# Kernel tuning notes

Hardware: AMD Instinct MI355X
Metric: run time of the kernel (lower is better)

The kernel has to match this reference:

```python
import jax, jax.numpy as jnp
from jax import lax
import numpy as np

N, B, P, D, DOUT, MAXDEG = 81920, 4096, 20, 128, 256, 8
EPS = 1e-5

def _bn(x, g, b):
    m = x.mean(0)
    v = x.var(0)
    return (x - m) / jnp.sqrt(v + EPS) * g + b

def setup_inputs() -> dict:
    key = jax.random.key(0)
    ks = jax.random.split(key, 24)
    s = 0.05
    return {
        'feat': jax.random.normal(ks[0], (N, D), jnp.float32),
        'intend': jax.random.normal(ks[1], (B, D), jnp.float32),
        'position_weight': jax.random.uniform(ks[2], (N,), jnp.float32),
        'nbr_idx': jax.random.randint(ks[3], (N, MAXDEG), 0, N),
        'deg': jax.random.randint(ks[4], (N,), 0, MAXDEG + 1),
        'last_nodes': jax.random.randint(ks[5], (B,), 0, N),
        # EOPA params
        'bn1_g': jnp.ones((D,), jnp.float32),
        'bn1_b': jnp.zeros((D,), jnp.float32),
        'W_ih': jax.random.normal(ks[6], (3 * D, D), jnp.float32) * s,
        'W_hh': jax.random.normal(ks[7], (3 * D, D), jnp.float32) * s,
        'b_ih': jax.random.normal(ks[8], (3 * D,), jnp.float32) * s,
        'b_hh': jax.random.normal(ks[9], (3 * D,), jnp.float32) * s,
        'W_self': jax.random.normal(ks[10], (D, D), jnp.float32) * s,
        'W_neigh': jax.random.normal(ks[11], (D, D), jnp.float32) * s,
        # AttnReadout params (hidden_dim == D)
        'bn2_g': jnp.ones((D,), jnp.float32),
        'bn2_b': jnp.zeros((D,), jnp.float32),
        'Wu': jax.random.normal(ks[12], (D, D), jnp.float32) * s,
        'Wv': jax.random.normal(ks[13], (D, D), jnp.float32) * s,
        'bv': jax.random.normal(ks[14], (D,), jnp.float32) * s,
        'Wi': jax.random.normal(ks[15], (D, D), jnp.float32) * s,
        'bi': jax.random.normal(ks[16], (D,), jnp.float32) * s,
        'We': jax.random.normal(ks[17], (D, 1), jnp.float32) * s,
        'Wout': jax.random.normal(ks[18], (DOUT, D), jnp.float32) * s,
    }

def reference(feat, intend, position_weight, nbr_idx, deg, last_nodes,
              bn1_g, bn1_b, W_ih, W_hh, b_ih, b_hh, W_self, W_neigh,
              bn2_g, bn2_b, Wu, Wv, bv, Wi, bi, We, Wout):
    # ---- EOPA: gather mailbox -> GRU over neighbors -> self + neigh mix ----
    h0 = _bn(feat, bn1_g, bn1_b)              # BatchNorm1d (batch stats)
    mail = h0[nbr_idx]                        # [N, MAXDEG, D] gather
    xs = jnp.moveaxis(mail, 0, 1)             # [MAXDEG, N, D]

    def gru_step(h, tx):
        t, x = tx
        gi = x @ W_ih.T + b_ih                # [N, 3D]
        gh = h @ W_hh.T + b_hh
        ir, iz, inn = jnp.split(gi, 3, axis=1)
        hr, hz, hn = jnp.split(gh, 3, axis=1)
        r = jax.nn.sigmoid(ir + hr)
        z = jax.nn.sigmoid(iz + hz)
        n = jnp.tanh(inn + r * hn)
        h_new = (1.0 - z) * n + z * h
        # freeze state past each node's true mailbox length (ragged GRU)
        h = jnp.where((t < deg)[:, None], h_new, h)
        return h, None

    neigh, _ = lax.scan(gru_step, jnp.zeros((N, D), feat.dtype),
                        (jnp.arange(MAXDEG), xs))
    rst = h0 @ W_self.T + neigh @ W_neigh.T   # [N, D], activation=None

    # ---- AttnReadout: segment softmax attention + segment sums ----
    h = _bn(rst, bn2_g, bn2_b)
    fu = (h @ Wu.T).reshape(B, P, D)
    fv = (intend @ Wv.T + bv)[:, None, :]         # broadcast_nodes
    fl = (h[last_nodes] @ Wi.T + bi)[:, None, :]  # broadcast_nodes
    e = (jax.nn.sigmoid(fu + fv + fl) @ We)[..., 0]   # [B, P]
    alpha = jax.nn.softmax(e, axis=1)[..., None]      # segment_softmax
    hg = h.reshape(B, P, D)
    rst_g = (hg * alpha).sum(axis=1) @ Wout.T         # segment_sum + fc_out
    pos = (hg * position_weight.reshape(B, P, 1)).sum(axis=1) @ Wout.T
    return rst_g, pos
```

## Files before the change

kernel.cpp:

```cpp
#include <hip/hip_runtime.h>

#define NN      81920
#define BB      4096
#define PP      20
#define DD      128
#define DOUTT   256
#define MAXDEGG 8
#define NBLK_H  320

using bf16x8 = __attribute__((ext_vector_type(8))) short;
using f32x4  = __attribute__((ext_vector_type(4))) float;
using u16x4  = __attribute__((ext_vector_type(4))) ushort;

__device__ __forceinline__ float b2f(ushort u) {
    union { unsigned u; float f; } v; v.u = ((unsigned)u) << 16; return v.f;
}
__device__ __forceinline__ ushort f2b(float f) {
    union { float f; unsigned u; } v; v.f = f;
    unsigned r = v.u + 0x7fffu + ((v.u >> 16) & 1u);
    return (ushort)(r >> 16);
}
__device__ __forceinline__ float sigm(float x) {
    return __fdividef(1.f, 1.f + __expf(-x));
}
__device__ __forceinline__ float tanh_fast(float x) {
    return 1.f - __fdividef(2.f, 1.f + __expf(2.f * x));
}
__device__ __forceinline__ f32x4 mfma16(bf16x8 a, bf16x8 b, f32x4 c) {
    return __builtin_amdgcn_mfma_f32_16x16x32_bf16(a, b, c, 0, 0, 0);
}
__device__ __forceinline__ bf16x8 pack8(float4 a, float4 b) {
    bf16x8 r;
    r[0] = (short)f2b(a.x); r[1] = (short)f2b(a.y);
    r[2] = (short)f2b(a.z); r[3] = (short)f2b(a.w);
    r[4] = (short)f2b(b.x); r[5] = (short)f2b(b.y);
    r[6] = (short)f2b(b.z); r[7] = (short)f2b(b.w);
    return r;
}
__device__ __forceinline__ bf16x8 ld8_bf(const ushort* p) { return *(const bf16x8*)p; }
__device__ __forceinline__ bf16x8 ld8_f32(const float* p) {
    return pack8(*(const float4*)p, *(const float4*)(p + 4));
}

__global__ __launch_bounds__(256) void stats_hist_k(const float* __restrict__ X,
                                                    const int* __restrict__ deg,
                                                    float* __restrict__ part,
                                                    int* __restrict__ blockHist) {
    const int tid = threadIdx.x;
    if (blockIdx.x < 640) {
        const int col  = tid & 127;
        const int half = tid >> 7;
        const long base = (long)blockIdx.x * 128 + (long)half * 64;
        float s = 0.f, q = 0.f;
        for (int i = 0; i < 64; ++i) {
            float x = X[(base + i) * 128 + col];
            s += x; q += x * x;
        }
        __shared__ float red[2][2][128];
        red[0][half][col] = s;
        red[1][half][col] = q;
        __syncthreads();
        if (tid < 128) {
            part[blockIdx.x * 128 + tid]             = red[0][0][tid] + red[0][1][tid];
            part[640 * 128 + blockIdx.x * 128 + tid] = red[1][0][tid] + red[1][1][tid];
        }
    } else {
        __shared__ int wh[4][9];
        const int hb = blockIdx.x - 640;
        const int w = tid >> 6, lane = tid & 63;
        int d = deg[hb * 256 + tid]; d = min(max(d, 0), 8);
#pragma unroll
        for (int c = 0; c < 9; ++c) {
            unsigned long long m = __ballot(d == c);
            if (lane == 0) wh[w][c] = __popcll(m);
        }
        __syncthreads();
        if (tid < 9) {
            int s = 0;
#pragma unroll
            for (int w2 = 0; w2 < 4; ++w2) s += wh[w2][tid];
            blockHist[hb * 9 + tid] = s;
        }
    }
}

__global__ __launch_bounds__(256) void bnfinal_scan_k(const float* __restrict__ part, int nparts,
                                                      const float* __restrict__ g,
                                                      const float* __restrict__ b,
                                                      float2* __restrict__ ss,
                                                      const int* __restrict__ blockHist,
                                                      int* __restrict__ blockBase) {
    const int t = threadIdx.x;
    if (blockIdx.x < 128) {
        const int c = blockIdx.x;
        float s = 0.f, q = 0.f;
        for (int i = t; i < nparts; i += 256) {
            s += part[(long)i * 128 + c];
            q += part[(long)(nparts + i) * 128 + c];
        }
#pragma unroll
        for (int off = 32; off > 0; off >>= 1) {
            s += __shfl_xor(s, off, 64);
            q += __shfl_xor(q, off, 64);
        }
        __shared__ float rs[4], rq[4];
        if ((t & 63) == 0) { rs[t >> 6] = s; rq[t >> 6] = q; }
        __syncthreads();
        if (t == 0) {
            s = rs[0] + rs[1] + rs[2] + rs[3];
            q = rq[0] + rq[1] + rq[2] + rq[3];
            const float inv_n = 1.f / (float)NN;
            float mean = s * inv_n;
            float var  = q * inv_n - mean * mean;
            float rstd = rsqrtf(var + 1e-5f);
            float sc = g[c] * rstd;
            ss[c] = make_float2(sc, b[c] - mean * sc);
        }
    } else {
        __shared__ int classTot[9], classStart[9];
        if (t < 9) {
            int s = 0;
            for (int b2 = 0; b2 < NBLK_H; ++b2) s += blockHist[b2 * 9 + t];
            classTot[t] = s;
        }
        __syncthreads();
        if (t == 0) {
            int acc = 0;
            for (int k = 0; k < 9; ++k) { classStart[k] = acc; acc += classTot[k]; }
        }
        __syncthreads();
        if (t < 9) {
            int acc = classStart[t];
            for (int b2 = 0; b2 < NBLK_H; ++b2) {
                blockBase[b2 * 9 + t] = acc;
                acc += blockHist[b2 * 9 + t];
            }
        }
    }
}

__global__ __launch_bounds__(256) void scatter_k(const int* __restrict__ deg,
                                                 const int* __restrict__ blockBase,
                                                 int* __restrict__ perm) {
    __shared__ int wh[4][9];
    __shared__ int wbase[4][9];
    const int t = threadIdx.x, w = t >> 6, lane = t & 63;
    const int i = blockIdx.x * 256 + t;
    int d = deg[i]; d = min(max(d, 0), 8);
    int lt = 0;
#pragma unroll
    for (int c = 0; c < 9; ++c) {
        unsigned long long m = __ballot(d == c);
        if (lane == 0) wh[w][c] = __popcll(m);
        if (d == c) lt = __popcll(m & ((1ull << lane) - 1ull));
    }
    __syncthreads();
    if (t < 36) {
        const int w2 = t / 9, c = t - w2 * 9;
        int s = blockBase[blockIdx.x * 9 + c];
        for (int k = 0; k < w2; ++k) s += wh[k][c];
        wbase[w2][c] = s;
    }
    __syncthreads();
    perm[wbase[w][d] + lt] = i;
}

template <int NCOL, int NWAVE, int KPARTS, bool A1F32, bool GATHER2, bool BIAS1,
          bool BIAS2, bool FOLD1, bool FOLD2, int OUTMODE>
__global__ __launch_bounds__(NWAVE * 64) void gemm_bt(
    const void* __restrict__ A1, const void* __restrict__ A2,
    const float* __restrict__ W1, const float* __restrict__ W2,
    const float* __restrict__ bias1, const float* __restrict__ bias2, int blim,
    const float2* __restrict__ ssW1, const float2* __restrict__ ssW2,
    const int* __restrict__ gidx, void* __restrict__ outv,
    float* __restrict__ part, int nparts,
    const float* __restrict__ fvl, const float* __restrict__ We,
    float* __restrict__ e) {
    constexpr int JT = NCOL / (16 * NWAVE);
    __shared__ float epart[8][64];
    const int tid = threadIdx.x;
    const int w   = tid >> 6;
    const int l   = tid & 63;
    const int l15 = l & 15;
    const int l4  = l >> 4;
    const int colbase = w * (NCOL / NWAVE);

    bf16x8 bfr[JT][KPARTS * 4];
    float bv[JT];
    float Wec[JT];
#pragma unroll
    for (int jl = 0; jl < JT; ++jl) {
        const int wrow = colbase + jl * 16 + l15;
        float fb = 0.f;
#pragma unroll
        for (int kp = 0; kp < KPARTS; ++kp) {
            const float* Wp = (kp == 0) ? W1 : W2;
            const float2* sp = (kp == 0) ? ssW1 : ssW2;
            const bool fold = (kp == 0) ? FOLD1 : FOLD2;
#pragma unroll
            for (int kt = 0; kt < 4; ++kt) {
                const float* wp = &Wp[(long)wrow * 128 + kt * 32 + l4 * 8];
                float4 a = *(const float4*)wp;
                float4 b4 = *(const float4*)(wp + 4);
                if (fold) {
                    const float* s = (const float*)(sp + kt * 32 + l4 * 8);
                    float4 s0 = *(const float4*)s, s1 = *(const float4*)(s + 4);
                    float4 s2 = *(const float4*)(s + 8), s3 = *(const float4*)(s + 12);
                    fb += s0.y * a.x + s0.w * a.y + s1.y * a.z + s1.w * a.w
                        + s2.y * b4.x + s2.w * b4.y + s3.y * b4.z + s3.w * b4.w;
                    a.x *= s0.x; a.y *= s0.z; a.z *= s1.x; a.w *= s1.z;
                    b4.x *= s2.x; b4.y *= s2.z; b4.z *= s3.x; b4.w *= s3.z;
                }
                bfr[jl][kp * 4 + kt] = pack8(a, b4);
            }
        }
        if (FOLD1 || FOLD2) {
            fb += __shfl_xor(fb, 16, 64);
            fb += __shfl_xor(fb, 32, 64);
        }
        if (BIAS1) fb += bias1[wrow];
        if (BIAS2) fb += (wrow < blim) ? bias2[wrow] : 0.f;
        bv[jl] = fb;
        if (OUTMODE == 3) Wec[jl] = We[wrow];
    }

    const int rowblk = blockIdx.x * 64;
    const f32x4 fz = {0.f, 0.f, 0.f, 0.f};
    float ssum[JT], sq[JT];
#pragma unroll
    for (int jl = 0; jl < JT; ++jl) { ssum[jl] = 0.f; sq[jl] = 0.f; }

#pragma unroll
    for (int it = 0; it < 4; ++it) {
        const int arow1 = rowblk + it * 16 + l15;
        bf16x8 afr[KPARTS * 4];
#pragma unroll
        for (int kt = 0; kt < 4; ++kt) {
            if (A1F32)
                afr[kt] = ld8_f32(&((const float*)A1)[(long)arow1 * 128 + kt * 32 + l4 * 8]);
            else
                afr[kt] = ld8_bf(&((const ushort*)A1)[(long)arow1 * 128 + kt * 32 + l4 * 8]);
        }
        if (KPARTS == 2) {
            const long arow2 = GATHER2 ? (long)gidx[arow1] : (long)arow1;
#pragma unroll
            for (int kt = 0; kt < 4; ++kt)
                afr[4 + kt] = ld8_bf(&((const ushort*)A2)[arow2 * 128 + kt * 32 + l4 * 8]);
        }
        f32x4 acc[JT];
#pragma unroll
        for (int jl = 0; jl < JT; ++jl) {
            acc[jl] = fz;
#pragma unroll
            for (int kk = 0; kk < KPARTS * 4; ++kk)
                acc[jl] = mfma16(afr[kk], bfr[jl][kk], acc[jl]);
        }
        float ps[4] = {0.f, 0.f, 0.f, 0.f};
#pragma unroll
        for (int jl = 0; jl < JT; ++jl) {
            const int col = colbase + jl * 16 + l15;
#pragma unroll
            for (int r = 0; r < 4; ++r) {
                const long orow = rowblk + it * 16 + l4 * 4 + r;
                float v = acc[jl][r] + bv[jl];
                if (OUTMODE == 0 || OUTMODE == 2)
                    ((ushort*)outv)[orow * NCOL + col] = f2b(v);
                if (OUTMODE == 1)
                    ((float*)outv)[orow * NCOL + col] = v;
                if (OUTMODE == 2) { ssum[jl] += v; sq[jl] += v * v; }
                if (OUTMODE == 3) {
                    const int b = (int)orow / PP;
                    ps[r] += sigm(v + fvl[(long)b * 128 + col]) * Wec[jl];
                }
            }
        }
        if (OUTMODE == 3) {
#pragma unroll
            for (int r = 0; r < 4; ++r) {
#pragma unroll
                for (int off = 1; off < 16; off <<= 1)
                    ps[r] += __shfl_xor(ps[r], off, 64);
            }
            if (l15 == 0) {
#pragma unroll
                for (int r = 0; r < 4; ++r)
                    epart[w][it * 16 + l4 * 4 + r] = ps[r];
            }
        }
    }
    if (OUTMODE == 2) {
#pragma unroll
        for (int jl = 0; jl < JT; ++jl) {
            float s = ssum[jl], q = sq[jl];
            s += __shfl_xor(s, 16, 64); s += __shfl_xor(s, 32, 64);
            q += __shfl_xor(q, 16, 64); q += __shfl_xor(q, 32, 64);
            if (l4 == 0) {
                const int col = colbase + jl * 16 + l15;
                part[(long)blockIdx.x * 128 + col] = s;
                part[(long)nparts * 128 + (long)blockIdx.x * 128 + col] = q;
            }
        }
    }
    if (OUTMODE == 3) {
        __syncthreads();
        if (tid < 64) {
            float s = 0.f;
#pragma unroll
            for (int w2 = 0; w2 < NWAVE; ++w2) s += epart[w2][tid];
            e[rowblk + tid] = s;
        }
    }
}

#define GLOAD(d0, d1, d2, ROW, TT)                                 \
    { const ushort* Gp_ = G + (long)nbrs[ROW][TT] * 384;           \
      d0 = *(const u16x4*)&Gp_[c0];                                \
      d1 = *(const u16x4*)&Gp_[c0 + 128];                          \
      d2 = *(const u16x4*)&Gp_[c0 + 256]; }

#define GRU_STEP(IT, Gv0, Gv1, Gv2)                                         \
    {                                                                       \
        const int row_ = (IT) * 16 + l15;                                   \
        const bool upd_ = (t < dreg[IT]);                                   \
        bf16x8 af0 = *(const bf16x8*)&hbuf[cur][row_][0 * 32 + l4 * 8];     \
        bf16x8 af1 = *(const bf16x8*)&hbuf[cur][row_][1 * 32 + l4 * 8];     \
        bf16x8 af2 = *(const bf16x8*)&hbuf[cur][row_][2 * 32 + l4 * 8];     \
        bf16x8 af3 = *(const bf16x8*)&hbuf[cur][row_][3 * 32 + l4 * 8];     \
        f32x4 ar = fz, az = fz, an = fz;                                    \
        ar = mfma16(bfr[0][0], af0, ar); az = mfma16(bfr[1][0], af0, az);   \
        an = mfma16(bfr[2][0], af0, an);                                    \
        ar = mfma16(bfr[0][1], af1, ar); az = mfma16(bfr[1][1], af1, az);   \
        an = mfma16(bfr[2][1], af1, an);                                    \
        ar = mfma16(bfr[0][2], af2, ar); az = mfma16(bfr[1][2], af2, az);   \
        an = mfma16(bfr[2][2], af2, an);                                    \
        ar = mfma16(bfr[0][3], af3, ar); az = mfma16(bfr[1][3], af3, az);   \
        an = mfma16(bfr[2][3], af3, an);                                    \
        const u16x4 hold_ = *(const u16x4*)&hbuf[cur][row_][c0];            \
        u16x4 hnew_;                                                        \
        _Pragma("unroll")                                                   \
        for (int r = 0; r < 4; ++r) {                                       \
            const float rr = sigm(b2f(Gv0[r]) + ar[r]);                     \
            const float zz = sigm(b2f(Gv1[r]) + az[r]);                     \
            const float nn = tanh_fast(b2f(Gv2[r]) + rr * (an[r] + bnN[r]));\
            const float hv = (1.f - zz) * nn + zz * b2f(hold_[r]);          \
            hnew_[r] = upd_ ? f2b(hv) : hold_[r];                           \
        }                                                                   \
        *(u16x4*)&hbuf[1 - cur][row_][c0] = hnew_;                          \
    }

__global__ __attribute__((amdgpu_flat_work_group_size(512, 512), amdgpu_waves_per_eu(4, 8)))
void gru_kernel(const ushort* __restrict__ G,
                const float* __restrict__ Whh,
                const float* __restrict__ bhh,
                const int* __restrict__ nbr_idx,
                const int* __restrict__ deg,
                const int* __restrict__ perm,
                ushort* __restrict__ neigh) {
    __shared__ alignas(16) ushort hbuf[2][64][136];
    __shared__ alignas(16) int nbrs[64][8];
    __shared__ int degs[64];
    __shared__ int nid[64];

    const int tid = threadIdx.x;
    const int l   = tid & 63;
    const int l15 = l & 15;
    const int l4  = l >> 4;
    const int blockRow = (gridDim.x - 1 - blockIdx.x) * 64;
    const int colbase = (tid >> 6) * 16;
    const int c0 = colbase + l4 * 4;

    if (tid < 64) nid[tid] = perm[blockRow + tid];
    {
        bf16x8 z = {0, 0, 0, 0, 0, 0, 0, 0};
        bf16x8* p = (bf16x8*)&hbuf[0][0][0];
        for (int i = tid; i < 64 * 136 / 8; i += 512) p[i] = z;
    }
    __syncthreads();
    nbrs[tid >> 3][tid & 7] = nbr_idx[(long)nid[tid >> 3] * 8 + (tid & 7)];
    if (tid < 64) degs[tid] = deg[nid[tid]];

    bf16x8 bfr[3][4];
#pragma unroll
    for (int g = 0; g < 3; ++g)
#pragma unroll
        for (int kt = 0; kt < 4; ++kt)
            bfr[g][kt] = ld8_f32(&Whh[(long)(g * 128 + colbase + l15) * 128 + kt * 32 + l4 * 8]);
    const f32x4 bnN = *(const f32x4*)&bhh[256 + c0];
    __syncthreads();

    int dreg[4];
#pragma unroll
    for (int it = 0; it < 4; ++it) dreg[it] = degs[it * 16 + l15];
    int dmax = degs[l];
#pragma unroll
    for (int off = 32; off > 0; off >>= 1) dmax = max(dmax, __shfl_xor(dmax, off, 64));
    dmax = __builtin_amdgcn_readfirstlane(dmax);

    const f32x4 fz = {0.f, 0.f, 0.f, 0.f};
    u16x4 p00, p01, p02, p10, p11, p12;
    GLOAD(p00, p01, p02, l15, 0);
    GLOAD(p10, p11, p12, 16 + l15, 0);

    int cur = 0;
    for (int t = 0; t < dmax; ++t) {
        u16x4 q20, q21, q22, q30, q31, q32;
        GLOAD(q20, q21, q22, 32 + l15, t);
        GLOAD(q30, q31, q32, 48 + l15, t);
        GRU_STEP(0, p00, p01, p02);
        GRU_STEP(1, p10, p11, p12);
        if (t + 1 < dmax) {
            GLOAD(p00, p01, p02, l15, t + 1);
            GLOAD(p10, p11, p12, 16 + l15, t + 1);
        }
        GRU_STEP(2, q20, q21, q22);
        GRU_STEP(3, q30, q31, q32);
        __syncthreads();
        cur ^= 1;
    }
    for (int idx = tid; idx < 64 * 16; idx += 512) {
        const int row = idx >> 4, ch = idx & 15;
        bf16x8* dst = (bf16x8*)(neigh + (long)nid[row] * 128);
        dst[ch] = *(const bf16x8*)&hbuf[cur][row][ch * 8];
    }
}

__global__ __launch_bounds__(256) void seg_k(const ushort* __restrict__ rst,
                                             const float* __restrict__ e,
                                             const float* __restrict__ pw,
                                             const float2* __restrict__ ss2,
                                             ushort* __restrict__ s12) {
    const int g = blockIdx.x * 2 + (threadIdx.x >> 7);
    const int c = threadIdx.x & 127;
    const float2 sc = ss2[c];
    float ev[PP];
    float m = -1e30f;
#pragma unroll
    for (int p = 0; p < PP; ++p) { ev[p] = e[g * PP + p]; m = fmaxf(m, ev[p]); }
    float sum = 0.f;
#pragma unroll
    for (int p = 0; p < PP; ++p) { ev[p] = __expf(ev[p] - m); sum += ev[p]; }
    const float inv = __fdividef(1.f, sum);
    float a1 = 0.f, a2 = 0.f;
#pragma unroll
    for (int p = 0; p < PP; ++p) {
        const int node = g * PP + p;
        const float hv = b2f(rst[(long)node * 128 + c]) * sc.x + sc.y;
        a1 += (ev[p] * inv) * hv;
        a2 += pw[node] * hv;
    }
    s12[(long)g * 128 + c]        = f2b(a1);
    s12[(long)(BB + g) * 128 + c] = f2b(a2);
}

extern "C" void kernel_launch(void* const* d_in, const int* in_sizes, int n_in,
                              void* d_out, int out_size, void* d_ws, size_t ws_size,
                              hipStream_t stream) {
    const float* feat    = (const float*)d_in[0];
    const float* intend  = (const float*)d_in[1];
    const float* pw      = (const float*)d_in[2];
    const int*   nbr_idx = (const int*)d_in[3];
    const int*   deg     = (const int*)d_in[4];
    const int*   last    = (const int*)d_in[5];
    const float* bn1_g   = (const float*)d_in[6];
    const float* bn1_b   = (const float*)d_in[7];
    const float* W_ih    = (const float*)d_in[8];
    const float* W_hh    = (const float*)d_in[9];
    const float* b_ih    = (const float*)d_in[10];
    const float* b_hh    = (const float*)d_in[11];
    const float* W_self  = (const float*)d_in[12];
    const float* W_neigh = (const float*)d_in[13];
    const float* bn2_g   = (const float*)d_in[14];
    const float* bn2_b   = (const float*)d_in[15];
    const float* Wu      = (const float*)d_in[16];
    const float* Wv      = (const float*)d_in[17];
    const float* bv      = (const float*)d_in[18];
    const float* Wi      = (const float*)d_in[19];
    const float* bi      = (const float*)d_in[20];
    const float* We      = (const float*)d_in[21];
    const float* Wout    = (const float*)d_in[22];
    float* out = (float*)d_out;
    char* ws = (char*)d_ws;

    ushort* G     = (ushort*)(ws + 0L);
    ushort* rst   = G;
    ushort* neigh = (ushort*)(ws + 62914560L);
    float*  fvl   = (float*)(ws + 83886080L);
    float*  e     = (float*)(ws + 85983232L);
    ushort* s12   = (ushort*)(ws + 86310912L);
    float*  part1 = (float*)(ws + 88408064L);
    float*  part2 = (float*)(ws + 89063424L);
    int*    perm  = (int*)(ws + 90374144L);
    float2* ss1   = (float2*)(ws + 90701824L);
    float2* ss2   = (float2*)(ws + 90702848L);
    int*    blockHist = (int*)(ws + 90703872L);
    int*    blockBase = (int*)(ws + 90715392L);

    stats_hist_k<<<960, 256, 0, stream>>>(feat, deg, part1, blockHist);
    bnfinal_scan_k<<<129, 256, 0, stream>>>(part1, 640, bn1_g, bn1_b, ss1,
                                            blockHist, blockBase);
    scatter_k<<<NBLK_H, 256, 0, stream>>>(deg, blockBase, perm);

    gemm_bt<384, 4, 1, true, false, true, true, true, false, 0><<<1280, 256, 0, stream>>>(
        feat, nullptr, W_ih, nullptr, b_ih, b_hh, 256, ss1, nullptr,
        nullptr, G, nullptr, 0, nullptr, nullptr, nullptr);

    gru_kernel<<<1280, 512, 0, stream>>>(G, W_hh, b_hh, nbr_idx, deg, perm, neigh);

    gemm_bt<128, 4, 2, true, false, false, false, true, false, 2><<<1280, 256, 0, stream>>>(
        feat, neigh, W_self, W_neigh, nullptr, nullptr, 0, ss1, nullptr,
        nullptr, rst, part2, 1280, nullptr, nullptr, nullptr);
    bnfinal_scan_k<<<128, 256, 0, stream>>>(part2, 1280, bn2_g, bn2_b, ss2,
                                            nullptr, nullptr);

    gemm_bt<128, 4, 2, true, true, true, true, false, true, 1><<<64, 256, 0, stream>>>(
        intend, rst, Wv, Wi, bv, bi, 128, nullptr, ss2,
        last, fvl, nullptr, 0, nullptr, nullptr, nullptr);

    gemm_bt<128, 4, 1, false, false, false, false, true, false, 3><<<1280, 256, 0, stream>>>(
        rst, nullptr, Wu, nullptr, nullptr, nullptr, 0, ss2, nullptr,
        nullptr, nullptr, nullptr, 0, fvl, We, e);

    seg_k<<<2048, 256, 0, stream>>>(rst, e, pw, ss2, s12);

    gemm_bt<256, 4, 1, false, false, false, false, false, false, 1><<<128, 256, 0, stream>>>(
        s12, nullptr, Wout, nullptr, nullptr, nullptr, 0, nullptr, nullptr,
        nullptr, out, nullptr, 0, nullptr, nullptr, nullptr);

    (void)in_sizes; (void)n_in; (void)out_size; (void)ws_size;
}
```

Measured before the change: 329.3 us.

## Fuse attention-score GEMM with segment softmax and weighted sums

Replaces the separate Wu GEMM kernel (which wrote per-node attention scores e) and the segment-reduction kernel with one kernel. Each block computes scores for 80 nodes (4 graphs), does the softmax in shared memory, then computes the attention-weighted and position-weighted sums. This removes a launch, the e buffer round trip, and gives the second rst read a chance to hit cache. In exchange the softmax is done serially by 4 threads, and each block has less parallelism per graph.

```diff
diff --git a/kernel.cpp b/kernel.cpp
--- a/kernel.cpp
+++ b/kernel.cpp
@@ -173,11 +173,8 @@
     const float* __restrict__ bias1, const float* __restrict__ bias2, int blim,
     const float2* __restrict__ ssW1, const float2* __restrict__ ssW2,
     const int* __restrict__ gidx, void* __restrict__ outv,
-    float* __restrict__ part, int nparts,
-    const float* __restrict__ fvl, const float* __restrict__ We,
-    float* __restrict__ e) {
+    float* __restrict__ part, int nparts) {
     constexpr int JT = NCOL / (16 * NWAVE);
-    __shared__ float epart[8][64];
     const int tid = threadIdx.x;
     const int w   = tid >> 6;
     const int l   = tid & 63;
@@ -187,7 +184,6 @@
 
     bf16x8 bfr[JT][KPARTS * 4];
     float bv[JT];
-    float Wec[JT];
 #pragma unroll
     for (int jl = 0; jl < JT; ++jl) {
         const int wrow = colbase + jl * 16 + l15;
@@ -221,7 +217,6 @@
         if (BIAS1) fb += bias1[wrow];
         if (BIAS2) fb += (wrow < blim) ? bias2[wrow] : 0.f;
         bv[jl] = fb;
-        if (OUTMODE == 3) Wec[jl] = We[wrow];
     }
 
     const int rowblk = blockIdx.x * 64;
@@ -255,7 +250,6 @@
             for (int kk = 0; kk < KPARTS * 4; ++kk)
                 acc[jl] = mfma16(afr[kk], bfr[jl][kk], acc[jl]);
         }
-        float ps[4] = {0.f, 0.f, 0.f, 0.f};
 #pragma unroll
         for (int jl = 0; jl < JT; ++jl) {
             const int col = colbase + jl * 16 + l15;
@@ -268,23 +262,6 @@
                 if (OUTMODE == 1)
                     ((float*)outv)[orow * NCOL + col] = v;
                 if (OUTMODE == 2) { ssum[jl] += v; sq[jl] += v * v; }
-                if (OUTMODE == 3) {
-                    const int b = (int)orow / PP;
-                    ps[r] += sigm(v + fvl[(long)b * 128 + col]) * Wec[jl];
-                }
-            }
-        }
-        if (OUTMODE == 3) {
-#pragma unroll
-            for (int r = 0; r < 4; ++r) {
-#pragma unroll
-                for (int off = 1; off < 16; off <<= 1)
-                    ps[r] += __shfl_xor(ps[r], off, 64);
-            }
-            if (l15 == 0) {
-#pragma unroll
-                for (int r = 0; r < 4; ++r)
-                    epart[w][it * 16 + l4 * 4 + r] = ps[r];
             }
         }
     }
@@ -299,15 +276,6 @@
                 part[(long)blockIdx.x * 128 + col] = s;
                 part[(long)nparts * 128 + (long)blockIdx.x * 128 + col] = q;
             }
-        }
-    }
-    if (OUTMODE == 3) {
-        __syncthreads();
-        if (tid < 64) {
-            float s = 0.f;
-#pragma unroll
-            for (int w2 = 0; w2 < NWAVE; ++w2) s += epart[w2][tid];
-            e[rowblk + tid] = s;
         }
     }
 }
@@ -424,32 +392,120 @@
     }
 }
 
-__global__ __launch_bounds__(256) void seg_k(const ushort* __restrict__ rst,
-                                             const float* __restrict__ e,
-                                             const float* __restrict__ pw,
-                                             const float2* __restrict__ ss2,
-                                             ushort* __restrict__ s12) {
-    const int g = blockIdx.x * 2 + (threadIdx.x >> 7);
-    const int c = threadIdx.x & 127;
-    const float2 sc = ss2[c];
-    float ev[PP];
-    float m = -1e30f;
-#pragma unroll
-    for (int p = 0; p < PP; ++p) { ev[p] = e[g * PP + p]; m = fmaxf(m, ev[p]); }
-    float sum = 0.f;
-#pragma unroll
-    for (int p = 0; p < PP; ++p) { ev[p] = __expf(ev[p] - m); sum += ev[p]; }
-    const float inv = __fdividef(1.f, sum);
-    float a1 = 0.f, a2 = 0.f;
-#pragma unroll
-    for (int p = 0; p < PP; ++p) {
-        const int node = g * PP + p;
-        const float hv = b2f(rst[(long)node * 128 + c]) * sc.x + sc.y;
-        a1 += (ev[p] * inv) * hv;
-        a2 += pw[node] * hv;
-    }
-    s12[(long)g * 128 + c]        = f2b(a1);
-    s12[(long)(BB + g) * 128 + c] = f2b(a2);
+__global__ __launch_bounds__(256) void seg_e_k(const ushort* __restrict__ rst,
+                                               const float* __restrict__ Wu,
+                                               const float2* __restrict__ ss2,
+                                               const float* __restrict__ fvl,
+                                               const float* __restrict__ We,
+                                               const float* __restrict__ pw,
+                                               ushort* __restrict__ s12) {
+    __shared__ float epart[4][80];
+    __shared__ float ash[80];
+    const int tid = threadIdx.x;
+    const int w   = tid >> 6;
+    const int l   = tid & 63;
+    const int l15 = l & 15;
+    const int l4  = l >> 4;
+    const int colbase = w * 32;
+    const int rowblk = blockIdx.x * 80;
+
+    bf16x8 bfr[2][4];
+    float bv[2], Wec[2];
+#pragma unroll
+    for (int jl = 0; jl < 2; ++jl) {
+        const int wrow = colbase + jl * 16 + l15;
+        float fb = 0.f;
+#pragma unroll
+        for (int kt = 0; kt < 4; ++kt) {
+            const float* wp = &Wu[(long)wrow * 128 + kt * 32 + l4 * 8];
+            float4 a = *(const float4*)wp;
+            float4 b4 = *(const float4*)(wp + 4);
+            const float* s = (const float*)(ss2 + kt * 32 + l4 * 8);
+            float4 s0 = *(const float4*)s, s1 = *(const float4*)(s + 4);
+            float4 s2 = *(const float4*)(s + 8), s3 = *(const float4*)(s + 12);
+            fb += s0.y * a.x + s0.w * a.y + s1.y * a.z + s1.w * a.w
+                + s2.y * b4.x + s2.w * b4.y + s3.y * b4.z + s3.w * b4.w;
+            a.x *= s0.x; a.y *= s0.z; a.z *= s1.x; a.w *= s1.z;
+            b4.x *= s2.x; b4.y *= s2.z; b4.z *= s3.x; b4.w *= s3.z;
+            bfr[jl][kt] = pack8(a, b4);
+        }
+        fb += __shfl_xor(fb, 16, 64);
+        fb += __shfl_xor(fb, 32, 64);
+        bv[jl] = fb;
+        Wec[jl] = We[wrow];
+    }
+
+    const f32x4 fz = {0.f, 0.f, 0.f, 0.f};
+#pragma unroll
+    for (int it = 0; it < 5; ++it) {
+        const int arow = rowblk + it * 16 + l15;
+        bf16x8 afr[4];
+#pragma unroll
+        for (int kt = 0; kt < 4; ++kt)
+            afr[kt] = ld8_bf(&rst[(long)arow * 128 + kt * 32 + l4 * 8]);
+        f32x4 acc[2];
+#pragma unroll
+        for (int jl = 0; jl < 2; ++jl) {
+            acc[jl] = fz;
+#pragma unroll
+            for (int kt = 0; kt < 4; ++kt)
+                acc[jl] = mfma16(afr[kt], bfr[jl][kt], acc[jl]);
+        }
+        float ps[4] = {0.f, 0.f, 0.f, 0.f};
+#pragma unroll
+        for (int jl = 0; jl < 2; ++jl) {
+            const int col = colbase + jl * 16 + l15;
+#pragma unroll
+            for (int r = 0; r < 4; ++r) {
+                const long orow = rowblk + it * 16 + l4 * 4 + r;
+                const float v = acc[jl][r] + bv[jl];
+                const int bg = (int)orow / PP;
+                ps[r] += sigm(v + fvl[(long)bg * 128 + col]) * Wec[jl];
+            }
+        }
+#pragma unroll
+        for (int r = 0; r < 4; ++r) {
+#pragma unroll
+            for (int off = 1; off < 16; off <<= 1)
+                ps[r] += __shfl_xor(ps[r], off, 64);
+        }
+        if (l15 == 0) {
+#pragma unroll
+            for (int r = 0; r < 4; ++r)
+                epart[w][it * 16 + l4 * 4 + r] = ps[r];
+        }
+    }
+    __syncthreads();
+    if (tid < 80)
+        ash[tid] = epart[0][tid] + epart[1][tid] + epart[2][tid] + epart[3][tid];
+    __syncthreads();
+    if (tid < 4) {
+        const int o = tid * PP;
+        float m = -1e30f;
+        for (int p = 0; p < PP; ++p) m = fmaxf(m, ash[o + p]);
+        float sum = 0.f;
+        for (int p = 0; p < PP; ++p) { ash[o + p] = __expf(ash[o + p] - m); sum += ash[o + p]; }
+        const float inv = __fdividef(1.f, sum);
+        for (int p = 0; p < PP; ++p) ash[o + p] *= inv;
+    }
+    __syncthreads();
+    const int c = tid & 127;
+    const float2 sc2 = ss2[c];
+#pragma unroll
+    for (int pass = 0; pass < 2; ++pass) {
+        const int gl = pass * 2 + (tid >> 7);
+        const int g = blockIdx.x * 4 + gl;
+        float a1 = 0.f, a2 = 0.f;
+#pragma unroll
+        for (int p = 0; p < PP; ++p) {
+            const int node = g * PP + p;
+            const float hv = b2f(rst[(long)node * 128 + c]) * sc2.x + sc2.y;
+            a1 += ash[gl * PP + p] * hv;
+            a2 += pw[node] * hv;
+        }
+        s12[(long)g * 128 + c]        = f2b(a1);
+        s12[(long)(BB + g) * 128 + c] = f2b(a2);
+    }
 }
 
 extern "C" void kernel_launch(void* const* d_in, const int* in_sizes, int n_in,
@@ -485,7 +541,6 @@
     ushort* rst   = G;
     ushort* neigh = (ushort*)(ws + 62914560L);
     float*  fvl   = (float*)(ws + 83886080L);
-    float*  e     = (float*)(ws + 85983232L);
     ushort* s12   = (ushort*)(ws + 86310912L);
     float*  part1 = (float*)(ws + 88408064L);
     float*  part2 = (float*)(ws + 89063424L);
@@ -502,29 +557,25 @@
 
     gemm_bt<384, 4, 1, true, false, true, true, true, false, 0><<<1280, 256, 0, stream>>>(
         feat, nullptr, W_ih, nullptr, b_ih, b_hh, 256, ss1, nullptr,
-        nullptr, G, nullptr, 0, nullptr, nullptr, nullptr);
+        nullptr, G, nullptr, 0);
 
     gru_kernel<<<1280, 512, 0, stream>>>(G, W_hh, b_hh, nbr_idx, deg, perm, neigh);
 
     gemm_bt<128, 4, 2, true, false, false, false, true, false, 2><<<1280, 256, 0, stream>>>(
         feat, neigh, W_self, W_neigh, nullptr, nullptr, 0, ss1, nullptr,
-        nullptr, rst, part2, 1280, nullptr, nullptr, nullptr);
+        nullptr, rst, part2, 1280);
     bnfinal_scan_k<<<128, 256, 0, stream>>>(part2, 1280, bn2_g, bn2_b, ss2,
                                             nullptr, nullptr);
 
     gemm_bt<128, 4, 2, true, true, true, true, false, true, 1><<<64, 256, 0, stream>>>(
         intend, rst, Wv, Wi, bv, bi, 128, nullptr, ss2,
-        last, fvl, nullptr, 0, nullptr, nullptr, nullptr);
-
-    gemm_bt<128, 4, 1, false, false, false, false, true, false, 3><<<1280, 256, 0, stream>>>(
-        rst, nullptr, Wu, nullptr, nullptr, nullptr, 0, ss2, nullptr,
-        nullptr, nullptr, nullptr, 0, fvl, We, e);
-
-    seg_k<<<2048, 256, 0, stream>>>(rst, e, pw, ss2, s12);
+        last, fvl, nullptr, 0);
+
+    seg_e_k<<<1024, 256, 0, stream>>>(rst, Wu, ss2, fvl, We, pw, s12);
 
     gemm_bt<256, 4, 1, false, false, false, false, false, false, 1><<<128, 256, 0, stream>>>(
         s12, nullptr, Wout, nullptr, nullptr, nullptr, 0, nullptr, nullptr,
-        nullptr, out, nullptr, 0, nullptr, nullptr, nullptr);
+        nullptr, out, nullptr, 0);
 
     (void)in_sizes; (void)n_in; (void)out_size; (void)ws_size;
 }
```

After: 325.7 us, median of 3. Within noise of the previous version (-1.1%).
